# Kernel optimization log

Hardware: AMD Instinct MI355X
Metric: run time of the kernel (lower is better)

## Reference

```python
import jax, jax.numpy as jnp
import numpy as np

N_HEADS = 32
N_KV_HEADS = 8
HEAD_DIM = 128
N_REP = N_HEADS // N_KV_HEADS
Q_SIZE = N_HEADS * HEAD_DIM        # 4096
K_SIZE = N_KV_HEADS * HEAD_DIM     # 1024


def setup_inputs() -> dict:
    key = jax.random.key(0)
    ks = jax.random.split(key, 5)
    B, T, D = 2, 2048, 4096
    x = jax.random.normal(ks[0], (B, T, D), dtype=jnp.float32)
    # complex freqs_cis split into real (cos) and imag (sin) parts, [T, head_dim/2]
    pos = jnp.arange(T, dtype=jnp.float32)[:, None]
    inv_freq = 1.0 / (10000.0 ** (jnp.arange(0, HEAD_DIM, 2, dtype=jnp.float32) / HEAD_DIM))
    ang = pos * inv_freq[None, :]
    freqs_cos = jnp.cos(ang)
    freqs_sin = jnp.sin(ang)
    w_qkv = jax.random.normal(ks[1], (Q_SIZE + 2 * K_SIZE, D), dtype=jnp.float32) * (D ** -0.5)
    wo_w = jax.random.normal(ks[2], (D, Q_SIZE), dtype=jnp.float32) * (Q_SIZE ** -0.5)
    return {"x": x, "freqs_cos": freqs_cos, "freqs_sin": freqs_sin, "w_qkv": w_qkv, "wo_w": wo_w}


def _apply_rotary(t, cos, sin):
    # t: [B, T, H, D]; cos/sin: [T, D/2] -> broadcast to [1, T, 1, D/2]
    tr = t.reshape(t.shape[:-1] + (HEAD_DIM // 2, 2))
    t0, t1 = tr[..., 0], tr[..., 1]
    c = cos[None, :, None, :]
    s = sin[None, :, None, :]
    o0 = t0 * c - t1 * s
    o1 = t0 * s + t1 * c
    return jnp.stack([o0, o1], axis=-1).reshape(t.shape)


def reference(x, freqs_cos, freqs_sin, w_qkv, wo_w):
    B, T, _ = x.shape
    qkv = jnp.einsum('btd,nd->btn', x, w_qkv)  # fused QKV GEMM
    q = qkv[..., :Q_SIZE].reshape(B, T, N_HEADS, HEAD_DIM)
    k = qkv[..., Q_SIZE:Q_SIZE + K_SIZE].reshape(B, T, N_KV_HEADS, HEAD_DIM)
    v = qkv[..., Q_SIZE + K_SIZE:].reshape(B, T, N_KV_HEADS, HEAD_DIM)
    q = _apply_rotary(q, freqs_cos, freqs_sin)
    k = _apply_rotary(k, freqs_cos, freqs_sin)
    # [B, H, T, D]
    q = q.transpose(0, 2, 1, 3)
    k = k.transpose(0, 2, 1, 3)
    v = v.transpose(0, 2, 1, 3)
    # GQA repeat_interleave along head dim
    k = jnp.repeat(k, N_REP, axis=1)
    v = jnp.repeat(v, N_REP, axis=1)
    scale = HEAD_DIM ** -0.5
    scores = jnp.einsum('bhqd,bhkd->bhqk', q, k) * scale
    causal = jnp.tril(jnp.ones((T, T), dtype=bool))
    scores = jnp.where(causal[None, None], scores, jnp.finfo(scores.dtype).min)
    attn = jax.nn.softmax(scores, axis=-1)
    y = jnp.einsum('bhqk,bhkd->bhqd', attn, v)
    y = y.transpose(0, 2, 1, 3).reshape(B, T, Q_SIZE)
    return jnp.einsum('btn,dn->btd', y, wo_w)
```

## Files before the change

kernel.cpp:

```cpp
#include <hip/hip_runtime.h>

typedef unsigned short u16t;
typedef unsigned int   u32t;
typedef __attribute__((ext_vector_type(8))) __bf16          bf16x8;
typedef __attribute__((ext_vector_type(8))) unsigned short  u16x8;
typedef __attribute__((ext_vector_type(4))) unsigned short  u16x4;
typedef __attribute__((ext_vector_type(4))) float           floatx4;

__device__ __forceinline__ u16t f2b(float f){
  u32t u = __builtin_bit_cast(u32t, f);
  u += 0x7fffu + ((u >> 16) & 1u);
  return (u16t)(u >> 16);
}
__device__ __forceinline__ float b2f(u16t h){
  return __builtin_bit_cast(float, (u32t)h << 16);
}
__device__ __forceinline__ void async16(const void* g, void* l){
  __builtin_amdgcn_global_load_lds((__attribute__((address_space(1))) void*)g,
                                   (__attribute__((address_space(3))) void*)l, 16, 0, 0);
}
__device__ __forceinline__ bf16x8 ldfrag(const u16t* p){
  return __builtin_bit_cast(bf16x8, *(const u16x8*)p);
}

__global__ __launch_bounds__(256)
void cvt_f32_bf16(const float* __restrict__ in, u16t* __restrict__ out, int n4){
  typedef __attribute__((ext_vector_type(4))) float f32x4;
  const f32x4* in4 = (const f32x4*)in;
  int stride = gridDim.x * blockDim.x;
  for (int i = blockIdx.x * blockDim.x + threadIdx.x; i < n4; i += stride){
    f32x4 v = in4[i];
    u16x4 o; o[0]=f2b(v[0]); o[1]=f2b(v[1]); o[2]=f2b(v[2]); o[3]=f2b(v[3]);
    *(u16x4*)(out + (size_t)i * 4) = o;
  }
}

#define MFMA16 __builtin_amdgcn_mfma_f32_16x16x32_bf16
template<int OUT_BF16>
__global__ __launch_bounds__(512, 2)
void gemm256(const u16t* __restrict__ A, const u16t* __restrict__ B,
             void* __restrict__ Cv, int M, int N, int K)
{
  (void)M;
  __shared__ u16t smem[65536];
  const int tid  = threadIdx.x;
  const int w    = tid >> 6, lane = tid & 63;
  const int lrow = lane & 15, quad = lane >> 4;
  const int wr   = w >> 2,  wc = w & 3;

  const int nwg  = (int)(gridDim.x * gridDim.y);
  const int flat = (int)(blockIdx.y * gridDim.x + blockIdx.x);
  const int q8 = nwg >> 3, r8 = nwg & 7, xcd = flat & 7, idx = flat >> 3;
  const int wg = (xcd < r8 ? xcd * (q8 + 1) : r8 * (q8 + 1) + (xcd - r8) * q8) + idx;
  const int m0 = (wg / (int)gridDim.x) * 256;
  const int n0 = (wg % (int)gridDim.x) * 256;

  const int srow = lane >> 3;
  const int scol = ((lane & 7) ^ srow) * 8;
  const u16t* gA = A + (size_t)(m0 + w * 8 + srow) * K + scol;
  const u16t* gB = B + (size_t)(n0 + w * 8 + srow) * K + scol;
  char* const ldsA = (char*)smem + w * 1024;
  char* const ldsB = (char*)smem + 65536 + w * 1024;
#define STA(h, i, buf, kt) async16(gA + (size_t)((h)*128 + (i)*64) * K + (kt)*64, \
                                   ldsA + (buf)*32768 + ((h)*2+(i))*8192)
#define STB(h, i, buf, kt) async16(gB + (size_t)((h)*128 + (i)*64) * K + (kt)*64, \
                                   ldsB + (buf)*32768 + ((h)*2+(i))*8192)

  const char* const sbb = (const char*)smem;
  const int c0   = ((quad ^ (lrow & 7)) * 16);
  const int aoff = (wr * 128 + lrow) * 128;
  const int boff = 65536 + (wc * 64 + lrow) * 128;

  floatx4 acc[8][4] = {};
  bf16x8 A0f[4][2], A1f[4][2], Bf0[2][2], Bf1[2][2];
  const int NT = K >> 6;

  STA(0,0,0,0); STA(0,1,0,0); STA(1,0,0,0); STA(1,1,0,0);
  STB(0,0,0,0); STB(0,1,0,0); STB(1,0,0,0); STB(1,1,0,0);
  STA(0,0,1,1); STA(0,1,1,1); STA(1,0,1,1); STA(1,1,1,1);
  STB(0,0,1,1); STB(0,1,1,1);
  asm volatile("s_waitcnt vmcnt(6)" ::: "memory");
  __builtin_amdgcn_sched_barrier(0);
  __builtin_amdgcn_s_barrier();

  for (int t = 0; t < NT; ++t){
    const int bsel = t & 1, nb = bsel ^ 1;
    const int bo = bsel * 32768;

#pragma unroll
    for (int mi = 0; mi < 4; ++mi){
      A0f[mi][0] = ldfrag((const u16t*)(sbb + bo + aoff + mi * 2048 + c0));
      A0f[mi][1] = ldfrag((const u16t*)(sbb + bo + aoff + mi * 2048 + (c0 ^ 64)));
    }
#pragma unroll
    for (int ni = 0; ni < 2; ++ni){
      Bf0[ni][0] = ldfrag((const u16t*)(sbb + bo + boff + ni * 2048 + c0));
      Bf0[ni][1] = ldfrag((const u16t*)(sbb + bo + boff + ni * 2048 + (c0 ^ 64)));
    }
    if (t + 1 < NT){ STB(1,0,nb,t+1); STB(1,1,nb,t+1); }
    __builtin_amdgcn_s_barrier();
    asm volatile("s_waitcnt lgkmcnt(0)" ::: "memory");
    __builtin_amdgcn_sched_barrier(0);
    __builtin_amdgcn_s_setprio(1);
#pragma unroll
    for (int mi = 0; mi < 4; ++mi)
#pragma unroll
      for (int ni = 0; ni < 2; ++ni){
        acc[mi][ni] = MFMA16(A0f[mi][0], Bf0[ni][0], acc[mi][ni], 0, 0, 0);
        acc[mi][ni] = MFMA16(A0f[mi][1], Bf0[ni][1], acc[mi][ni], 0, 0, 0);
      }
    __builtin_amdgcn_s_setprio(0);
    __builtin_amdgcn_sched_barrier(0);
    __builtin_amdgcn_s_barrier();

#pragma unroll
    for (int mi = 0; mi < 4; ++mi){
      A1f[mi][0] = ldfrag((const u16t*)(sbb + bo + aoff + (4 + mi) * 2048 + c0));
      A1f[mi][1] = ldfrag((const u16t*)(sbb + bo + aoff + (4 + mi) * 2048 + (c0 ^ 64)));
    }
    if (t + 2 < NT){ STA(0,0,bsel,t+2); STA(0,1,bsel,t+2); }
    __builtin_amdgcn_s_barrier();
    asm volatile("s_waitcnt lgkmcnt(0)" ::: "memory");
    __builtin_amdgcn_sched_barrier(0);
    __builtin_amdgcn_s_setprio(1);
#pragma unroll
    for (int mi = 0; mi < 4; ++mi)
#pragma unroll
      for (int ni = 0; ni < 2; ++ni){
        acc[4+mi][ni] = MFMA16(A1f[mi][0], Bf0[ni][0], acc[4+mi][ni], 0, 0, 0);
        acc[4+mi][ni] = MFMA16(A1f[mi][1], Bf0[ni][1], acc[4+mi][ni], 0, 0, 0);
      }
    __builtin_amdgcn_s_setprio(0);
    __builtin_amdgcn_sched_barrier(0);
    __builtin_amdgcn_s_barrier();

#pragma unroll
    for (int ni = 0; ni < 2; ++ni){
      Bf1[ni][0] = ldfrag((const u16t*)(sbb + bo + boff + (2 + ni) * 2048 + c0));
      Bf1[ni][1] = ldfrag((const u16t*)(sbb + bo + boff + (2 + ni) * 2048 + (c0 ^ 64)));
    }
    if (t + 2 < NT){ STA(1,0,bsel,t+2); STA(1,1,bsel,t+2); }
    __builtin_amdgcn_s_barrier();
    asm volatile("s_waitcnt lgkmcnt(0)" ::: "memory");
    __builtin_amdgcn_sched_barrier(0);
    __builtin_amdgcn_s_setprio(1);
#pragma unroll
    for (int mi = 0; mi < 4; ++mi)
#pragma unroll
      for (int ni = 0; ni < 2; ++ni){
        acc[mi][2+ni] = MFMA16(A0f[mi][0], Bf1[ni][0], acc[mi][2+ni], 0, 0, 0);
        acc[mi][2+ni] = MFMA16(A0f[mi][1], Bf1[ni][1], acc[mi][2+ni], 0, 0, 0);
      }
    __builtin_amdgcn_s_setprio(0);
    __builtin_amdgcn_sched_barrier(0);
    __builtin_amdgcn_s_barrier();

    if (t + 2 < NT){ STB(0,0,bsel,t+2); STB(0,1,bsel,t+2); }
    __builtin_amdgcn_s_barrier();
    __builtin_amdgcn_s_setprio(1);
#pragma unroll
    for (int mi = 0; mi < 4; ++mi)
#pragma unroll
      for (int ni = 0; ni < 2; ++ni){
        acc[4+mi][2+ni] = MFMA16(A1f[mi][0], Bf1[ni][0], acc[4+mi][2+ni], 0, 0, 0);
        acc[4+mi][2+ni] = MFMA16(A1f[mi][1], Bf1[ni][1], acc[4+mi][2+ni], 0, 0, 0);
      }
    __builtin_amdgcn_s_setprio(0);
    __builtin_amdgcn_sched_barrier(0);
    if (t + 2 < NT) asm volatile("s_waitcnt vmcnt(6)" ::: "memory");
    else            asm volatile("s_waitcnt vmcnt(0)" ::: "memory");
    __builtin_amdgcn_sched_barrier(0);
    __builtin_amdgcn_s_barrier();
  }

#pragma unroll
  for (int mi = 0; mi < 8; ++mi)
#pragma unroll
    for (int ni = 0; ni < 4; ++ni)
#pragma unroll
      for (int r = 0; r < 4; ++r){
        int row = m0 + wr * 128 + mi * 16 + quad * 4 + r;
        int col = n0 + wc * 64 + ni * 16 + lrow;
        float v = acc[mi][ni][r];
        if (OUT_BF16) ((u16t*)Cv)[(size_t)row * N + col] = f2b(v);
        else          ((float*)Cv)[(size_t)row * N + col] = v;
      }
#undef STA
#undef STB
}

__global__ __launch_bounds__(256)
void rope_qk(const u16t* __restrict__ qkvb, const float* __restrict__ cosp,
             const float* __restrict__ sinp, u16t* __restrict__ qr, u16t* __restrict__ kr)
{
  const int row = blockIdx.x;
  const int b = row >> 11, t = row & 2047;
  const u16t* src = qkvb + (size_t)row * 6144;
  for (int p = threadIdx.x; p < 2560; p += 256){
    u32t both = *(const u32t*)(src + 2 * p);
    float t0 = b2f((u16t)(both & 0xffff));
    float t1 = b2f((u16t)(both >> 16));
    int j = p & 63;
    float c = cosp[t * 64 + j], s = sinp[t * 64 + j];
    float o0 = t0 * c - t1 * s;
    float o1 = t0 * s + t1 * c;
    u32t packed = (u32t)f2b(o0) | ((u32t)f2b(o1) << 16);
    if (p < 2048){
      int h = p >> 6;
      *(u32t*)(qr + (((size_t)(b * 32 + h) * 2048 + t) * 128 + 2 * j)) = packed;
    } else {
      int kh = (p - 2048) >> 6;
      *(u32t*)(kr + (((size_t)(b * 8 + kh) * 2048 + t) * 128 + 2 * j)) = packed;
    }
  }
}

__global__ __launch_bounds__(256)
void vtrans(const u16t* __restrict__ qkvb, u16t* __restrict__ vt)
{
  __shared__ u16t sV[64 * 128];
  const int tid = threadIdx.x;
  const int blk = blockIdx.x;
  const int tile = blk & 31, kvh = (blk >> 5) & 7, b = blk >> 8;
  const int t0 = tile * 64;
  const size_t srcbase = (size_t)(b * 2048 + t0) * 6144 + 5120 + kvh * 128;
#pragma unroll
  for (int it = 0; it < 4; ++it){
    int task = it * 256 + tid;
    int rrow = task >> 4, cb = task & 15;
    *(u16x8*)&sV[rrow * 128 + cb * 8] =
        *(const u16x8*)(qkvb + srcbase + (size_t)rrow * 6144 + cb * 8);
  }
  __syncthreads();
  const size_t dstbase = (size_t)((b * 8 + kvh) * 128) * 2048 + t0;
#pragma unroll
  for (int it = 0; it < 4; ++it){
    int task = it * 256 + tid;
    int tc = task & 7, d = task >> 3;
    u16x8 v;
#pragma unroll
    for (int j = 0; j < 8; ++j) v[j] = sV[(tc * 8 + j) * 128 + d];
    *(u16x8*)(vt + dstbase + (size_t)d * 2048 + tc * 8) = v;
  }
}

__global__ __launch_bounds__(256)
void attn_fwd(const u16t* __restrict__ Qg, const u16t* __restrict__ Kg,
              const u16t* __restrict__ Vt, u16t* __restrict__ Y)
{
  __shared__ u16t smem[37376];
  u16t* sP = smem + 32768;

  const int tid  = threadIdx.x;
  const int wave = tid >> 6, lane = tid & 63;
  const int lrow = lane & 15, quad = lane >> 4;
  const int qt = 31 - (int)blockIdx.y;
  const int q0 = qt * 64;
  const int bh = blockIdx.x;
  const int b = bh >> 5, h = bh & 31, kvh = h >> 2;
  const float qscale = 0.088388347648318447f * 1.4426950408889634f;

  bf16x8 aq[4];
  const size_t qbase = ((size_t)bh * 2048 + q0 + wave * 16) * 128;
#pragma unroll
  for (int kk = 0; kk < 4; ++kk)
    aq[kk] = ldfrag(Qg + qbase + (size_t)lrow * 128 + (kk * 4 + quad) * 8);

  const size_t kbase = ((size_t)(b * 8 + kvh) * 2048) * 128;
  const size_t vbase = ((size_t)(b * 8 + kvh) * 128) * 2048;

#define STAGEKV(kt_, bs_) {                                                     \
    const int k0_ = (kt_) * 64;                                                 \
    char* dK = (char*)smem + (bs_) * 16384;                                     \
    char* dV = (char*)smem + 32768 + (bs_) * 16384;                             \
    _Pragma("unroll")                                                           \
    for (int r = 0; r < 4; ++r){                                                \
      const int dc = r * 4 + wave;                                              \
      async16(Kg + kbase + (size_t)(k0_ + lane) * 128 + dc * 8, dK + dc * 1024);\
    }                                                                           \
    _Pragma("unroll")                                                           \
    for (int r = 0; r < 4; ++r){                                                \
      const int kvc = r * 2 + (wave >> 1);                                      \
      const int dd  = (wave & 1) * 64 + lane;                                   \
      async16(Vt + vbase + (size_t)dd * 2048 + k0_ + kvc * 8,                   \
              dV + kvc * 2048 + (wave & 1) * 1024);                             \
    } }

  float mi[4] = {-1e30f, -1e30f, -1e30f, -1e30f};
  float li[4] = {0.f, 0.f, 0.f, 0.f};
  floatx4 o[8] = {};
  const int qrow_base = q0 + wave * 16 + quad * 4;
  const int ktiles = qt + 1;

  STAGEKV(0, 0);

  for (int kt = 0; kt < ktiles; ++kt){
    const int bsel = kt & 1;
    const int k0 = kt * 64;
    if (kt + 1 < ktiles){
      STAGEKV(kt + 1, bsel ^ 1);
      asm volatile("s_waitcnt vmcnt(8)" ::: "memory");
    } else {
      asm volatile("s_waitcnt vmcnt(0)" ::: "memory");
    }
    __builtin_amdgcn_sched_barrier(0);
    __builtin_amdgcn_s_barrier();

    const u16t* cK = smem + bsel * 8192;
    const u16t* cV = smem + 16384 + bsel * 8192;

    floatx4 s[4] = {};
    __builtin_amdgcn_s_setprio(1);
#pragma unroll
    for (int kk = 0; kk < 4; ++kk){
#pragma unroll
      for (int nt = 0; nt < 4; ++nt){
        bf16x8 bk = ldfrag(&cK[((kk * 4 + quad) * 64 + nt * 16 + lrow) * 8]);
        s[nt] = __builtin_amdgcn_mfma_f32_16x16x32_bf16(aq[kk], bk, s[nt], 0, 0, 0);
      }
    }
    __builtin_amdgcn_s_setprio(0);

    float tt[4][4];
#pragma unroll
    for (int nt = 0; nt < 4; ++nt)
#pragma unroll
      for (int r = 0; r < 4; ++r)
        tt[nt][r] = s[nt][r] * qscale;
    if (kt == ktiles - 1){
#pragma unroll
      for (int nt = 0; nt < 4; ++nt){
        int kc = k0 + nt * 16 + lrow;
#pragma unroll
        for (int r = 0; r < 4; ++r)
          if (kc > qrow_base + r) tt[nt][r] = -1e30f;
      }
    }

    float rmax[4];
#pragma unroll
    for (int r = 0; r < 4; ++r)
      rmax[r] = fmaxf(fmaxf(tt[0][r], tt[1][r]), fmaxf(tt[2][r], tt[3][r]));
#pragma unroll
    for (int off = 1; off < 16; off <<= 1){
#pragma unroll
      for (int r = 0; r < 4; ++r)
        rmax[r] = fmaxf(rmax[r], __shfl_xor(rmax[r], off, 64));
    }
    float alpha[4];
#pragma unroll
    for (int r = 0; r < 4; ++r){
      float mn = fmaxf(mi[r], rmax[r]);
      alpha[r] = __builtin_amdgcn_exp2f(mi[r] - mn);
      mi[r] = mn;
    }
    float lsum[4] = {0.f, 0.f, 0.f, 0.f};
#pragma unroll
    for (int nt = 0; nt < 4; ++nt)
#pragma unroll
      for (int r = 0; r < 4; ++r){
        float e = __builtin_amdgcn_exp2f(tt[nt][r] - mi[r]);
        lsum[r] += e;
        sP[(wave * 16 + quad * 4 + r) * 72 + nt * 16 + lrow] = f2b(e);
      }
#pragma unroll
    for (int off = 1; off < 16; off <<= 1){
#pragma unroll
      for (int r = 0; r < 4; ++r)
        lsum[r] += __shfl_xor(lsum[r], off, 64);
    }
#pragma unroll
    for (int r = 0; r < 4; ++r) li[r] = li[r] * alpha[r] + lsum[r];
#pragma unroll
    for (int nt = 0; nt < 8; ++nt){
      o[nt][0] *= alpha[0]; o[nt][1] *= alpha[1];
      o[nt][2] *= alpha[2]; o[nt][3] *= alpha[3];
    }

    __builtin_amdgcn_s_setprio(1);
#pragma unroll
    for (int kk = 0; kk < 2; ++kk){
      bf16x8 ap = ldfrag(&sP[(wave * 16 + lrow) * 72 + kk * 32 + quad * 8]);
#pragma unroll
      for (int nt = 0; nt < 8; ++nt){
        bf16x8 bv = ldfrag(&cV[((kk * 4 + quad) * 128 + nt * 16 + lrow) * 8]);
        o[nt] = __builtin_amdgcn_mfma_f32_16x16x32_bf16(ap, bv, o[nt], 0, 0, 0);
      }
    }
    __builtin_amdgcn_s_setprio(0);
    __builtin_amdgcn_sched_barrier(0);
    __builtin_amdgcn_s_barrier();
  }
#undef STAGEKV

#pragma unroll
  for (int r = 0; r < 4; ++r){
    int t = q0 + wave * 16 + quad * 4 + r;
    float inv = 1.0f / li[r];
    size_t ybase = ((size_t)(b * 2048 + t)) * 4096 + h * 128;
#pragma unroll
    for (int nt = 0; nt < 8; ++nt)
      Y[ybase + nt * 16 + lrow] = f2b(o[nt][r] * inv);
  }
}

extern "C" void kernel_launch(void* const* d_in, const int* in_sizes, int n_in,
                              void* d_out, int out_size, void* d_ws, size_t ws_size,
                              hipStream_t stream)
{
  (void)in_sizes; (void)n_in; (void)out_size; (void)ws_size;
  const float* x    = (const float*)d_in[0];
  const float* fc   = (const float*)d_in[1];
  const float* fs   = (const float*)d_in[2];
  const float* wqkv = (const float*)d_in[3];
  const float* wo   = (const float*)d_in[4];
  float* out = (float*)d_out;

  char* ws = (char*)d_ws;
  u16t* xb    = (u16t*)(ws);
  u16t* wqkvb = (u16t*)(ws + 33554432);
  u16t* wob   = (u16t*)(ws + 83886080);
  u16t* qkvb  = (u16t*)(ws + 117440512);
  u16t* qr    = (u16t*)(ws + 167772160);
  u16t* kr    = (u16t*)(ws + 201326592);
  u16t* vt    = (u16t*)(ws + 209715200);
  u16t* yb    = xb;

  cvt_f32_bf16<<<4096, 256, 0, stream>>>(x,    xb,    16777216 / 4);
  cvt_f32_bf16<<<4096, 256, 0, stream>>>(wqkv, wqkvb, 25165824 / 4);
  cvt_f32_bf16<<<4096, 256, 0, stream>>>(wo,   wob,   16777216 / 4);
  gemm256<1><<<dim3(24, 16), 512, 0, stream>>>(xb, wqkvb, qkvb, 4096, 6144, 4096);
  rope_qk<<<4096, 256, 0, stream>>>(qkvb, fc, fs, qr, kr);
  vtrans<<<512, 256, 0, stream>>>(qkvb, vt);
  attn_fwd<<<dim3(64, 32), 256, 0, stream>>>(qr, kr, vt, yb);
  gemm256<0><<<dim3(16, 16), 512, 0, stream>>>(yb, wob, out, 4096, 4096, 4096);
}
```

Before: 772.0 us.

## Add 256x192-tile GEMM kernel for QKV projection to fix wave quantization

Adds a gemm192 kernel that computes 256x192 output tiles, with the matching LDS layout and its own interleaved load/MFMA schedule. The QKV projection now launches a 32x16 grid instead of the 24x16 grid of 256x256 tiles. The aim is to spread the 6144-wide output more evenly across the CUs and cut the partially filled last wave. The cost is smaller tiles, so less operand reuse per tile and more redundant A-matrix traffic.

```diff
diff --git a/kernel.cpp b/kernel.cpp
--- a/kernel.cpp
+++ b/kernel.cpp
@@ -36,6 +36,7 @@
 }
 
 #define MFMA16 __builtin_amdgcn_mfma_f32_16x16x32_bf16
+
 template<int OUT_BF16>
 __global__ __launch_bounds__(512, 2)
 void gemm256(const u16t* __restrict__ A, const u16t* __restrict__ B,
@@ -184,6 +185,151 @@
         float v = acc[mi][ni][r];
         if (OUT_BF16) ((u16t*)Cv)[(size_t)row * N + col] = f2b(v);
         else          ((float*)Cv)[(size_t)row * N + col] = v;
+      }
+#undef STA
+#undef STB
+}
+
+__global__ __launch_bounds__(512, 2)
+void gemm192(const u16t* __restrict__ A, const u16t* __restrict__ B,
+             u16t* __restrict__ C, int M, int N, int K)
+{
+  (void)M;
+  __shared__ u16t smem[57344];
+  const int tid  = threadIdx.x;
+  const int w    = tid >> 6, lane = tid & 63;
+  const int lrow = lane & 15, quad = lane >> 4;
+  const int wr   = w >> 2,  wc = w & 3;
+
+  const int nwg  = (int)(gridDim.x * gridDim.y);
+  const int flat = (int)(blockIdx.y * gridDim.x + blockIdx.x);
+  const int q8 = nwg >> 3, r8 = nwg & 7, xcd = flat & 7, idx = flat >> 3;
+  const int wg = (xcd < r8 ? xcd * (q8 + 1) : r8 * (q8 + 1) + (xcd - r8) * q8) + idx;
+  const int m0 = (wg / (int)gridDim.x) * 256;
+  const int n0 = (wg % (int)gridDim.x) * 192;
+
+  const int srow = lane >> 3;
+  const int scol = ((lane & 7) ^ srow) * 8;
+  const u16t* gA = A + (size_t)(m0 + w * 8 + srow) * K + scol;
+  const u16t* gB = B + (size_t)(n0 + w * 8 + srow) * K + scol;
+  char* const ldsA = (char*)smem + w * 1024;
+  char* const ldsB = (char*)smem + 65536 + w * 1024;
+#define STA(h, i, buf, kt) async16(gA + (size_t)((h)*128 + (i)*64) * K + (kt)*64, \
+                                   ldsA + (buf)*32768 + ((h)*2+(i))*8192)
+#define STB(c, buf, kt)    async16(gB + (size_t)((c)*64) * K + (kt)*64, \
+                                   ldsB + (buf)*24576 + (c)*8192)
+
+  const char* const sbb = (const char*)smem;
+  const int c0   = ((quad ^ (lrow & 7)) * 16);
+  const int aoff = (wr * 128 + lrow) * 128;
+  const int boff = 65536 + (wc * 48 + lrow) * 128;
+
+  floatx4 acc[8][3] = {};
+  bf16x8 A0f[4][2], A1f[4][2], Bf0[2][2], Bf1[2];
+  const int NT = K >> 6;
+
+  STA(0,0,0,0); STA(0,1,0,0);
+  STB(0,0,0);   STB(1,0,0);   STB(2,0,0);
+  STA(1,0,0,0); STA(1,1,0,0);
+  STA(0,0,1,1); STA(0,1,1,1);
+  STB(0,1,1);   STB(1,1,1);
+  STA(1,0,1,1); STA(1,1,1,1);
+  asm volatile("s_waitcnt vmcnt(6)" ::: "memory");
+  __builtin_amdgcn_sched_barrier(0);
+  __builtin_amdgcn_s_barrier();
+
+  for (int t = 0; t < NT; ++t){
+    const int bsel = t & 1, nb = bsel ^ 1;
+    const int ao = bsel * 32768, bo = bsel * 24576;
+
+#pragma unroll
+    for (int mi = 0; mi < 4; ++mi){
+      A0f[mi][0] = ldfrag((const u16t*)(sbb + ao + aoff + mi * 2048 + c0));
+      A0f[mi][1] = ldfrag((const u16t*)(sbb + ao + aoff + mi * 2048 + (c0 ^ 64)));
+    }
+#pragma unroll
+    for (int ni = 0; ni < 2; ++ni){
+      Bf0[ni][0] = ldfrag((const u16t*)(sbb + bo + boff + ni * 2048 + c0));
+      Bf0[ni][1] = ldfrag((const u16t*)(sbb + bo + boff + ni * 2048 + (c0 ^ 64)));
+    }
+    if (t + 1 < NT){ STB(2,nb,t+1); }
+    __builtin_amdgcn_s_barrier();
+    asm volatile("s_waitcnt lgkmcnt(0)" ::: "memory");
+    __builtin_amdgcn_sched_barrier(0);
+    __builtin_amdgcn_s_setprio(1);
+#pragma unroll
+    for (int mi = 0; mi < 4; ++mi)
+#pragma unroll
+      for (int ni = 0; ni < 2; ++ni){
+        acc[mi][ni] = MFMA16(A0f[mi][0], Bf0[ni][0], acc[mi][ni], 0, 0, 0);
+        acc[mi][ni] = MFMA16(A0f[mi][1], Bf0[ni][1], acc[mi][ni], 0, 0, 0);
+      }
+    __builtin_amdgcn_s_setprio(0);
+    __builtin_amdgcn_sched_barrier(0);
+    __builtin_amdgcn_s_barrier();
+
+#pragma unroll
+    for (int mi = 0; mi < 4; ++mi){
+      A1f[mi][0] = ldfrag((const u16t*)(sbb + ao + aoff + (4 + mi) * 2048 + c0));
+      A1f[mi][1] = ldfrag((const u16t*)(sbb + ao + aoff + (4 + mi) * 2048 + (c0 ^ 64)));
+    }
+    if (t + 2 < NT){ STA(0,0,bsel,t+2); STA(0,1,bsel,t+2); }
+    __builtin_amdgcn_s_barrier();
+    asm volatile("s_waitcnt lgkmcnt(0)" ::: "memory");
+    __builtin_amdgcn_sched_barrier(0);
+    __builtin_amdgcn_s_setprio(1);
+#pragma unroll
+    for (int mi = 0; mi < 4; ++mi)
+#pragma unroll
+      for (int ni = 0; ni < 2; ++ni){
+        acc[4+mi][ni] = MFMA16(A1f[mi][0], Bf0[ni][0], acc[4+mi][ni], 0, 0, 0);
+        acc[4+mi][ni] = MFMA16(A1f[mi][1], Bf0[ni][1], acc[4+mi][ni], 0, 0, 0);
+      }
+    __builtin_amdgcn_s_setprio(0);
+    __builtin_amdgcn_sched_barrier(0);
+    __builtin_amdgcn_s_barrier();
+
+    Bf1[0] = ldfrag((const u16t*)(sbb + bo + boff + 2 * 2048 + c0));
+    Bf1[1] = ldfrag((const u16t*)(sbb + bo + boff + 2 * 2048 + (c0 ^ 64)));
+    if (t + 2 < NT){ STA(1,0,bsel,t+2); STA(1,1,bsel,t+2); }
+    __builtin_amdgcn_s_barrier();
+    asm volatile("s_waitcnt lgkmcnt(0)" ::: "memory");
+    __builtin_amdgcn_sched_barrier(0);
+    __builtin_amdgcn_s_setprio(1);
+#pragma unroll
+    for (int mi = 0; mi < 4; ++mi){
+      acc[mi][2] = MFMA16(A0f[mi][0], Bf1[0], acc[mi][2], 0, 0, 0);
+      acc[mi][2] = MFMA16(A0f[mi][1], Bf1[1], acc[mi][2], 0, 0, 0);
+    }
+    __builtin_amdgcn_s_setprio(0);
+    __builtin_amdgcn_sched_barrier(0);
+    __builtin_amdgcn_s_barrier();
+
+    if (t + 2 < NT){ STB(0,bsel,t+2); STB(1,bsel,t+2); }
+    __builtin_amdgcn_s_barrier();
+    __builtin_amdgcn_s_setprio(1);
+#pragma unroll
+    for (int mi = 0; mi < 4; ++mi){
+      acc[4+mi][2] = MFMA16(A1f[mi][0], Bf1[0], acc[4+mi][2], 0, 0, 0);
+      acc[4+mi][2] = MFMA16(A1f[mi][1], Bf1[1], acc[4+mi][2], 0, 0, 0);
+    }
+    __builtin_amdgcn_s_setprio(0);
+    __builtin_amdgcn_sched_barrier(0);
+    if (t + 2 < NT) asm volatile("s_waitcnt vmcnt(6)" ::: "memory");
+    else            asm volatile("s_waitcnt vmcnt(0)" ::: "memory");
+    __builtin_amdgcn_sched_barrier(0);
+    __builtin_amdgcn_s_barrier();
+  }
+
+#pragma unroll
+  for (int mi = 0; mi < 8; ++mi)
+#pragma unroll
+    for (int ni = 0; ni < 3; ++ni)
+#pragma unroll
+      for (int r = 0; r < 4; ++r){
+        int row = m0 + wr * 128 + mi * 16 + quad * 4 + r;
+        int col = n0 + wc * 48 + ni * 16 + lrow;
+        C[(size_t)row * N + col] = f2b(acc[mi][ni][r]);
       }
 #undef STA
 #undef STB
@@ -429,7 +575,7 @@
   cvt_f32_bf16<<<4096, 256, 0, stream>>>(x,    xb,    16777216 / 4);
   cvt_f32_bf16<<<4096, 256, 0, stream>>>(wqkv, wqkvb, 25165824 / 4);
   cvt_f32_bf16<<<4096, 256, 0, stream>>>(wo,   wob,   16777216 / 4);
-  gemm256<1><<<dim3(24, 16), 512, 0, stream>>>(xb, wqkvb, qkvb, 4096, 6144, 4096);
+  gemm192<<<dim3(32, 16), 512, 0, stream>>>(xb, wqkvb, qkvb, 4096, 6144, 4096);
   rope_qk<<<4096, 256, 0, stream>>>(qkvb, fc, fs, qr, kr);
   vtrans<<<512, 256, 0, stream>>>(qkvb, vt);
   attn_fwd<<<dim3(64, 32), 256, 0, stream>>>(qr, kr, vt, yb);
```

Result: faster. 740.3 us (-4.1%).
